# Kernel tuning notes

Hardware: AMD Instinct MI355X
Metric: run time of the kernel (lower is better)

The kernel has to match this reference:

```python
import jax, jax.numpy as jnp
import numpy as np
import math

STAGE_NUM = 10
K = 8
C = 256
KAPPA = 20.0


def _l2norm(x, axis):
    return x / (1e-06 + jnp.linalg.norm(x, axis=axis, keepdims=True))


def setup_inputs() -> dict:
    key = jax.random.key(0)
    k1, k2 = jax.random.split(key)
    support_feature = jax.random.normal(k1, (16, C, 128, 128), dtype=jnp.float32)
    mu = jax.random.normal(k2, (1, C, K), dtype=jnp.float32) * math.sqrt(2.0 / K)
    mu = _l2norm(mu, axis=1)  # matches mu.normal_(0, sqrt(2/k)) then _l2norm(dim=1)
    return {"support_feature": support_feature, "mu": mu}


def _em(x, mu0):
    # x: [b, c, n]; mu0: [b, c, k]
    b, c, n = x.shape

    def step(i, carry):
        mu, _ = carry
        # Kernel: kappa * x^T @ mu -> [b, n, k]
        z = jax.nn.softmax(KAPPA * jnp.einsum('bcn,bck->bnk', x, mu), axis=2)
        z_ = z / (1e-06 + z.sum(axis=1, keepdims=True))  # normalize over n
        mu = jnp.einsum('bcn,bnk->bck', x, z_)           # mu update
        mu = _l2norm(mu, axis=1)
        return (mu, z_)

    z_init = jnp.zeros((b, n, K), dtype=x.dtype)
    mu, z_ = jax.lax.fori_loop(0, STAGE_NUM, step, (mu0, z_init))
    return mu.transpose(0, 2, 1), z_  # mu: [b, k, c]


def reference(support_feature, mu):
    b, c, h, w = support_feature.shape
    x = support_feature.reshape(b, c, h * w)
    mu_b = jnp.broadcast_to(mu, (b, c, K))
    # Original runs EM entirely under torch.no_grad()
    mu_f, z_ = jax.lax.stop_gradient(_em(x, mu_b))
    # prototypes in original are list of mu_f[:, i, :, None, None]; return stacked mu_f
    return (mu_f, z_)
```

## Files before the change

### kernel.cpp

```cpp
#include <hip/hip_runtime.h>
#include <hip/hip_fp16.h>
#include <cstdint>
#include <cstddef>

#define NB 16
#define NC 256
#define NK 8
#define NN 16384
#define NSTAGE 10
#define FKAPPA 20.0f
#define NT 64
#define TPB 2
#define NBLK 128

__global__ __launch_bounds__(256) void k_init_mu(const float* __restrict__ mu_in,
                                                 float* __restrict__ mu_cur) {
    int i = blockIdx.x * 256 + threadIdx.x;
    mu_cur[i] = mu_in[i & (NC * NK - 1)];
}

template <bool WRITE_Z>
__global__ __launch_bounds__(256) void k_stage(const float* __restrict__ x,
                                               const float* __restrict__ mu,
                                               float* __restrict__ part,
                                               float* __restrict__ cspart,
                                               float* __restrict__ zraw) {
    const int b    = blockIdx.x >> 7;
    const int nt2  = blockIdx.x & (NBLK - 1);
    const int t    = threadIdx.x;
    const int lane = t & 63;
    const int wv   = t >> 6;

    __shared__ __align__(16) __half xt[NC][66];
    __shared__ __align__(16) float  smu[NC * NK];
    __shared__ __align__(16) float  dz[NT][12];

    for (int i = t; i < NC * NK; i += 256) smu[i] = mu[b * NC * NK + i];

    const int nl = (lane & 15) * 4;
    const int cg = lane >> 4;

    float a2[NK];
    float csk[NK];
    #pragma unroll
    for (int k = 0; k < NK; k++) { a2[k] = 0.f; csk[k] = 0.f; }

    for (int g = 0; g < TPB; ++g) {
        const int n0 = (nt2 * TPB + g) * NT;
        __syncthreads();
        if (t < NT * 12 / 4)
            reinterpret_cast<float4*>(dz)[t] = make_float4(0.f, 0.f, 0.f, 0.f);
        __syncthreads();

        const float* xp = x + (size_t)b * NC * NN + n0 + nl;
        float acc[4][NK];
        #pragma unroll
        for (int i = 0; i < 4; i++)
            #pragma unroll
            for (int k = 0; k < NK; k++) acc[i][k] = 0.f;

        #pragma unroll 8
        for (int ci = 0; ci < 16; ++ci) {
            const int c = wv * 64 + ci * 4 + cg;
            const float4 xv = *reinterpret_cast<const float4*>(xp + (size_t)c * NN);
            *reinterpret_cast<__half2*>(&xt[c][nl])     = __floats2half2_rn(xv.x, xv.y);
            *reinterpret_cast<__half2*>(&xt[c][nl + 2]) = __floats2half2_rn(xv.z, xv.w);
            const float4 m0 = *reinterpret_cast<const float4*>(&smu[c * NK]);
            const float4 m1 = *reinterpret_cast<const float4*>(&smu[c * NK + 4]);
            acc[0][0] += xv.x * m0.x; acc[0][1] += xv.x * m0.y; acc[0][2] += xv.x * m0.z; acc[0][3] += xv.x * m0.w;
            acc[0][4] += xv.x * m1.x; acc[0][5] += xv.x * m1.y; acc[0][6] += xv.x * m1.z; acc[0][7] += xv.x * m1.w;
            acc[1][0] += xv.y * m0.x; acc[1][1] += xv.y * m0.y; acc[1][2] += xv.y * m0.z; acc[1][3] += xv.y * m0.w;
            acc[1][4] += xv.y * m1.x; acc[1][5] += xv.y * m1.y; acc[1][6] += xv.y * m1.z; acc[1][7] += xv.y * m1.w;
            acc[2][0] += xv.z * m0.x; acc[2][1] += xv.z * m0.y; acc[2][2] += xv.z * m0.z; acc[2][3] += xv.z * m0.w;
            acc[2][4] += xv.z * m1.x; acc[2][5] += xv.z * m1.y; acc[2][6] += xv.z * m1.z; acc[2][7] += xv.z * m1.w;
            acc[3][0] += xv.w * m0.x; acc[3][1] += xv.w * m0.y; acc[3][2] += xv.w * m0.z; acc[3][3] += xv.w * m0.w;
            acc[3][4] += xv.w * m1.x; acc[3][5] += xv.w * m1.y; acc[3][6] += xv.w * m1.z; acc[3][7] += xv.w * m1.w;
        }

        #pragma unroll
        for (int m = 16; m <= 32; m <<= 1)
            #pragma unroll
            for (int i = 0; i < 4; i++)
                #pragma unroll
                for (int k = 0; k < NK; k++) acc[i][k] += __shfl_xor(acc[i][k], m, 64);

        if (lane < 16) {
            #pragma unroll
            for (int i = 0; i < 4; i++)
                #pragma unroll
                for (int k = 0; k < NK; k++) atomicAdd(&dz[nl + i][k], acc[i][k]);
        }
        __syncthreads();

        if (t < NT) {
            float l[NK];
            float mx = -1e30f;
            #pragma unroll
            for (int k = 0; k < NK; k++) { l[k] = FKAPPA * dz[t][k]; mx = fmaxf(mx, l[k]); }
            float s = 0.f;
            #pragma unroll
            for (int k = 0; k < NK; k++) { l[k] = __expf(l[k] - mx); s += l[k]; }
            const float inv = 1.f / s;
            #pragma unroll
            for (int k = 0; k < NK; k++) { l[k] *= inv; dz[t][k] = l[k]; }
            if (WRITE_Z) {
                float* zp = zraw + ((size_t)b * NN + n0 + t) * NK;
                *reinterpret_cast<float4*>(zp)     = make_float4(l[0], l[1], l[2], l[3]);
                *reinterpret_cast<float4*>(zp + 4) = make_float4(l[4], l[5], l[6], l[7]);
            }
            #pragma unroll
            for (int off = 32; off > 0; off >>= 1)
                #pragma unroll
                for (int k = 0; k < NK; k++) l[k] += __shfl_down(l[k], off, 64);
            #pragma unroll
            for (int k = 0; k < NK; k++) csk[k] += l[k];
        }
        __syncthreads();

        #pragma unroll 8
        for (int j = 0; j < NT / 2; ++j) {
            const __half2 xh = *reinterpret_cast<const __half2*>(&xt[t][2 * j]);
            const float2 xf = __half22float2(xh);
            const float4 za0 = *reinterpret_cast<const float4*>(&dz[2 * j][0]);
            const float4 za1 = *reinterpret_cast<const float4*>(&dz[2 * j][4]);
            const float4 zb0 = *reinterpret_cast<const float4*>(&dz[2 * j + 1][0]);
            const float4 zb1 = *reinterpret_cast<const float4*>(&dz[2 * j + 1][4]);
            a2[0] += xf.x * za0.x + xf.y * zb0.x;
            a2[1] += xf.x * za0.y + xf.y * zb0.y;
            a2[2] += xf.x * za0.z + xf.y * zb0.z;
            a2[3] += xf.x * za0.w + xf.y * zb0.w;
            a2[4] += xf.x * za1.x + xf.y * zb1.x;
            a2[5] += xf.x * za1.y + xf.y * zb1.y;
            a2[6] += xf.x * za1.z + xf.y * zb1.z;
            a2[7] += xf.x * za1.w + xf.y * zb1.w;
        }
    }

    float* pp = part + (size_t)blockIdx.x * (NC * NK) + t * NK;
    *reinterpret_cast<float4*>(pp)     = make_float4(a2[0], a2[1], a2[2], a2[3]);
    *reinterpret_cast<float4*>(pp + 4) = make_float4(a2[4], a2[5], a2[6], a2[7]);
    if (t == 0) {
        #pragma unroll
        for (int k = 0; k < NK; k++) cspart[blockIdx.x * NK + k] = csk[k];
    }
}

__global__ __launch_bounds__(256) void k_reduce(const float* __restrict__ part,
                                                const float* __restrict__ cspart,
                                                float* __restrict__ num,
                                                float* __restrict__ colsum) {
    const int b  = blockIdx.x >> 3;
    const int cg = blockIdx.x & 7;
    const int t  = threadIdx.x;
    const int ck = cg * 256 + t;

    float s = 0.f;
    const float* p = part + (size_t)b * NBLK * (NC * NK) + ck;
    #pragma unroll 8
    for (int g = 0; g < NBLK; ++g) s += p[(size_t)g * (NC * NK)];
    num[b * (NC * NK) + ck] = s;

    __shared__ float cred[2][NK];
    if (cg == 0 && t < NBLK) {
        const float4 u0 = *reinterpret_cast<const float4*>(&cspart[(b * NBLK + t) * NK]);
        const float4 u1 = *reinterpret_cast<const float4*>(&cspart[(b * NBLK + t) * NK + 4]);
        float v[NK] = {u0.x, u0.y, u0.z, u0.w, u1.x, u1.y, u1.z, u1.w};
        #pragma unroll
        for (int off = 32; off > 0; off >>= 1)
            #pragma unroll
            for (int k = 0; k < NK; k++) v[k] += __shfl_down(v[k], off, 64);
        if ((t & 63) == 0)
            #pragma unroll
            for (int k = 0; k < NK; k++) cred[t >> 6][k] = v[k];
    }
    __syncthreads();
    if (cg == 0 && t < NK) colsum[b * NK + t] = cred[0][t] + cred[1][t];
}

__global__ __launch_bounds__(256) void k_newmu(const float* __restrict__ num,
                                               const float* __restrict__ colsum,
                                               float* __restrict__ mu_out) {
    const int b = blockIdx.x;
    const int t = threadIdx.x;
    float inv[NK];
    #pragma unroll
    for (int k = 0; k < NK; k++) inv[k] = 1.f / (1e-6f + colsum[b * NK + k]);

    const float4 v0 = *reinterpret_cast<const float4*>(num + (size_t)b * NC * NK + t * NK);
    const float4 v1 = *reinterpret_cast<const float4*>(num + (size_t)b * NC * NK + t * NK + 4);
    float v[NK] = {v0.x * inv[0], v0.y * inv[1], v0.z * inv[2], v0.w * inv[3],
                   v1.x * inv[4], v1.y * inv[5], v1.z * inv[6], v1.w * inv[7]};

    float sq[NK];
    #pragma unroll
    for (int k = 0; k < NK; k++) sq[k] = v[k] * v[k];
    #pragma unroll
    for (int off = 32; off > 0; off >>= 1)
        #pragma unroll
        for (int k = 0; k < NK; k++) sq[k] += __shfl_down(sq[k], off, 64);

    __shared__ float red[4][NK];
    const int wave = t >> 6, lane = t & 63;
    if (lane == 0)
        #pragma unroll
        for (int k = 0; k < NK; k++) red[wave][k] = sq[k];
    __syncthreads();
    __shared__ float scale[NK];
    if (t < NK) {
        const float tot = red[0][t] + red[1][t] + red[2][t] + red[3][t];
        scale[t] = 1.f / (1e-6f + sqrtf(tot));
    }
    __syncthreads();
    #pragma unroll
    for (int k = 0; k < NK; k++) v[k] *= scale[k];
    *reinterpret_cast<float4*>(mu_out + (size_t)b * NC * NK + t * NK)     = make_float4(v[0], v[1], v[2], v[3]);
    *reinterpret_cast<float4*>(mu_out + (size_t)b * NC * NK + t * NK + 4) = make_float4(v[4], v[5], v[6], v[7]);
}

__global__ __launch_bounds__(256) void k_write_mu(const float* __restrict__ mu,
                                                  float* __restrict__ out) {
    const int i = blockIdx.x * 256 + threadIdx.x;
    const int b = i >> 11, r = i & 2047;
    const int k = r >> 8, c = r & 255;
    out[i] = mu[(size_t)b * NC * NK + c * NK + k];
}

__global__ __launch_bounds__(256) void k_write_z(const float* __restrict__ colsum,
                                                 float* __restrict__ out1) {
    const int i = blockIdx.x * 256 + threadIdx.x;
    const int b = i >> 12;
    const int n4 = (i & 4095) * 4;
    float inv[NK];
    #pragma unroll
    for (int k = 0; k < NK; k++) inv[k] = 1.f / (1e-6f + colsum[b * NK + k]);

    float4* p = reinterpret_cast<float4*>(out1 + ((size_t)b * NN + n4) * NK);
    #pragma unroll
    for (int j = 0; j < 4; ++j) {
        float4 a = p[2 * j], c = p[2 * j + 1];
        a.x *= inv[0]; a.y *= inv[1]; a.z *= inv[2]; a.w *= inv[3];
        c.x *= inv[4]; c.y *= inv[5]; c.z *= inv[6]; c.w *= inv[7];
        p[2 * j] = a; p[2 * j + 1] = c;
    }
}

extern "C" void kernel_launch(void* const* d_in, const int* in_sizes, int n_in,
                              void* d_out, int out_size, void* d_ws, size_t ws_size,
                              hipStream_t stream) {
    const float* x     = (const float*)d_in[0];
    const float* mu_in = (const float*)d_in[1];
    float* out  = (float*)d_out;
    float* out1 = out + NB * NK * NC;
    char* ws = (char*)d_ws;

    const size_t PART_BYTES = (size_t)NB * NBLK * NC * NK * 4;
    const size_t CSP_BYTES  = (size_t)NB * NBLK * NK * 4;
    const size_t NUM_BYTES  = (size_t)NB * NC * NK * 4;
    const size_t CS_BYTES   = (size_t)NB * NK * 4;

    float* part   = (float*)ws;
    float* cspart = (float*)(ws + PART_BYTES);
    float* num    = (float*)(ws + PART_BYTES + CSP_BYTES);
    float* colsum = (float*)(ws + PART_BYTES + CSP_BYTES + NUM_BYTES);
    float* mu_a   = (float*)(ws + PART_BYTES + CSP_BYTES + NUM_BYTES + CS_BYTES);

    k_init_mu<<<NB * NC * NK / 256, 256, 0, stream>>>(mu_in, mu_a);

    for (int s = 0; s < NSTAGE; ++s) {
        if (s == NSTAGE - 1)
            k_stage<true><<<NB * NBLK, 256, 0, stream>>>(x, mu_a, part, cspart, out1);
        else
            k_stage<false><<<NB * NBLK, 256, 0, stream>>>(x, mu_a, part, cspart, out1);
        k_reduce<<<NB * 8, 256, 0, stream>>>(part, cspart, num, colsum);
        k_newmu<<<NB, 256, 0, stream>>>(num, colsum, mu_a);
    }

    k_write_mu<<<NB * NK * NC / 256, 256, 0, stream>>>(mu_a, out);
    k_write_z<<<NB * NN / 4 / 256, 256, 0, stream>>>(colsum, out1);
}
```

Measured before the change: 1.688 ms.

## Double stage block to 512 threads, prefetch x loads, replace LDS atomics with per-wave partials

Each stage block now runs 512 threads (8 waves). Each wave covers 32 channels, and all eight float4 x loads are issued up front before the compute. The LDS atomicAdd reduction of logits is replaced by per-wave partial buffers that the softmax threads sum. The second matmul is split across two thread halves over n, which doubles the partial buffer and the reduce kernel's loop. This trades more LDS use and twice the reduction traffic for more memory parallelism and no atomics.

```diff
diff --git a/kernel.cpp b/kernel.cpp
--- a/kernel.cpp
+++ b/kernel.cpp
@@ -20,11 +20,11 @@
 }
 
 template <bool WRITE_Z>
-__global__ __launch_bounds__(256) void k_stage(const float* __restrict__ x,
-                                               const float* __restrict__ mu,
-                                               float* __restrict__ part,
-                                               float* __restrict__ cspart,
-                                               float* __restrict__ zraw) {
+__global__ __launch_bounds__(512, 4) void k_stage(const float* __restrict__ x,
+                                                  const float* __restrict__ mu,
+                                                  float* __restrict__ part,
+                                                  float* __restrict__ cspart,
+                                                  float* __restrict__ zraw) {
     const int b    = blockIdx.x >> 7;
     const int nt2  = blockIdx.x & (NBLK - 1);
     const int t    = threadIdx.x;
@@ -33,48 +33,53 @@
 
     __shared__ __align__(16) __half xt[NC][66];
     __shared__ __align__(16) float  smu[NC * NK];
+    __shared__ __align__(16) float  dzp[8][NT][9];
     __shared__ __align__(16) float  dz[NT][12];
 
-    for (int i = t; i < NC * NK; i += 256) smu[i] = mu[b * NC * NK + i];
+    reinterpret_cast<float4*>(smu)[t] =
+        reinterpret_cast<const float4*>(mu + (size_t)b * NC * NK)[t];
 
     const int nl = (lane & 15) * 4;
     const int cg = lane >> 4;
-
-    float a2[NK];
-    float csk[NK];
+    const int c2 = t & 255;
+    const int nh = t >> 8;
+
+    float a2[NK], csk[NK];
     #pragma unroll
     for (int k = 0; k < NK; k++) { a2[k] = 0.f; csk[k] = 0.f; }
 
     for (int g = 0; g < TPB; ++g) {
         const int n0 = (nt2 * TPB + g) * NT;
         __syncthreads();
-        if (t < NT * 12 / 4)
-            reinterpret_cast<float4*>(dz)[t] = make_float4(0.f, 0.f, 0.f, 0.f);
-        __syncthreads();
 
         const float* xp = x + (size_t)b * NC * NN + n0 + nl;
+        float4 xv[8];
+        #pragma unroll
+        for (int ci = 0; ci < 8; ++ci)
+            xv[ci] = *reinterpret_cast<const float4*>(xp + (size_t)(wv * 32 + ci * 4 + cg) * NN);
+
         float acc[4][NK];
         #pragma unroll
         for (int i = 0; i < 4; i++)
             #pragma unroll
             for (int k = 0; k < NK; k++) acc[i][k] = 0.f;
 
-        #pragma unroll 8
-        for (int ci = 0; ci < 16; ++ci) {
-            const int c = wv * 64 + ci * 4 + cg;
-            const float4 xv = *reinterpret_cast<const float4*>(xp + (size_t)c * NN);
-            *reinterpret_cast<__half2*>(&xt[c][nl])     = __floats2half2_rn(xv.x, xv.y);
-            *reinterpret_cast<__half2*>(&xt[c][nl + 2]) = __floats2half2_rn(xv.z, xv.w);
+        #pragma unroll
+        for (int ci = 0; ci < 8; ++ci) {
+            const int c = wv * 32 + ci * 4 + cg;
+            const float4 v = xv[ci];
+            *reinterpret_cast<__half2*>(&xt[c][nl])     = __floats2half2_rn(v.x, v.y);
+            *reinterpret_cast<__half2*>(&xt[c][nl + 2]) = __floats2half2_rn(v.z, v.w);
             const float4 m0 = *reinterpret_cast<const float4*>(&smu[c * NK]);
             const float4 m1 = *reinterpret_cast<const float4*>(&smu[c * NK + 4]);
-            acc[0][0] += xv.x * m0.x; acc[0][1] += xv.x * m0.y; acc[0][2] += xv.x * m0.z; acc[0][3] += xv.x * m0.w;
-            acc[0][4] += xv.x * m1.x; acc[0][5] += xv.x * m1.y; acc[0][6] += xv.x * m1.z; acc[0][7] += xv.x * m1.w;
-            acc[1][0] += xv.y * m0.x; acc[1][1] += xv.y * m0.y; acc[1][2] += xv.y * m0.z; acc[1][3] += xv.y * m0.w;
-            acc[1][4] += xv.y * m1.x; acc[1][5] += xv.y * m1.y; acc[1][6] += xv.y * m1.z; acc[1][7] += xv.y * m1.w;
-            acc[2][0] += xv.z * m0.x; acc[2][1] += xv.z * m0.y; acc[2][2] += xv.z * m0.z; acc[2][3] += xv.z * m0.w;
-            acc[2][4] += xv.z * m1.x; acc[2][5] += xv.z * m1.y; acc[2][6] += xv.z * m1.z; acc[2][7] += xv.z * m1.w;
-            acc[3][0] += xv.w * m0.x; acc[3][1] += xv.w * m0.y; acc[3][2] += xv.w * m0.z; acc[3][3] += xv.w * m0.w;
-            acc[3][4] += xv.w * m1.x; acc[3][5] += xv.w * m1.y; acc[3][6] += xv.w * m1.z; acc[3][7] += xv.w * m1.w;
+            acc[0][0] += v.x * m0.x; acc[0][1] += v.x * m0.y; acc[0][2] += v.x * m0.z; acc[0][3] += v.x * m0.w;
+            acc[0][4] += v.x * m1.x; acc[0][5] += v.x * m1.y; acc[0][6] += v.x * m1.z; acc[0][7] += v.x * m1.w;
+            acc[1][0] += v.y * m0.x; acc[1][1] += v.y * m0.y; acc[1][2] += v.y * m0.z; acc[1][3] += v.y * m0.w;
+            acc[1][4] += v.y * m1.x; acc[1][5] += v.y * m1.y; acc[1][6] += v.y * m1.z; acc[1][7] += v.y * m1.w;
+            acc[2][0] += v.z * m0.x; acc[2][1] += v.z * m0.y; acc[2][2] += v.z * m0.z; acc[2][3] += v.z * m0.w;
+            acc[2][4] += v.z * m1.x; acc[2][5] += v.z * m1.y; acc[2][6] += v.z * m1.z; acc[2][7] += v.z * m1.w;
+            acc[3][0] += v.w * m0.x; acc[3][1] += v.w * m0.y; acc[3][2] += v.w * m0.z; acc[3][3] += v.w * m0.w;
+            acc[3][4] += v.w * m1.x; acc[3][5] += v.w * m1.y; acc[3][6] += v.w * m1.z; acc[3][7] += v.w * m1.w;
         }
 
         #pragma unroll
@@ -88,7 +93,7 @@
             #pragma unroll
             for (int i = 0; i < 4; i++)
                 #pragma unroll
-                for (int k = 0; k < NK; k++) atomicAdd(&dz[nl + i][k], acc[i][k]);
+                for (int k = 0; k < NK; k++) dzp[wv][nl + i][k] = acc[i][k];
         }
         __syncthreads();
 
@@ -96,7 +101,13 @@
             float l[NK];
             float mx = -1e30f;
             #pragma unroll
-            for (int k = 0; k < NK; k++) { l[k] = FKAPPA * dz[t][k]; mx = fmaxf(mx, l[k]); }
+            for (int k = 0; k < NK; k++) {
+                float s = dzp[0][t][k];
+                #pragma unroll
+                for (int w = 1; w < 8; ++w) s += dzp[w][t][k];
+                l[k] = FKAPPA * s;
+                mx = fmaxf(mx, l[k]);
+            }
             float s = 0.f;
             #pragma unroll
             for (int k = 0; k < NK; k++) { l[k] = __expf(l[k] - mx); s += l[k]; }
@@ -118,8 +129,9 @@
         __syncthreads();
 
         #pragma unroll 8
-        for (int j = 0; j < NT / 2; ++j) {
-            const __half2 xh = *reinterpret_cast<const __half2*>(&xt[t][2 * j]);
+        for (int jj = 0; jj < 16; ++jj) {
+            const int j = nh * 16 + jj;
+            const __half2 xh = *reinterpret_cast<const __half2*>(&xt[c2][2 * j]);
             const float2 xf = __half22float2(xh);
             const float4 za0 = *reinterpret_cast<const float4*>(&dz[2 * j][0]);
             const float4 za1 = *reinterpret_cast<const float4*>(&dz[2 * j][4]);
@@ -136,7 +148,7 @@
         }
     }
 
-    float* pp = part + (size_t)blockIdx.x * (NC * NK) + t * NK;
+    float* pp = part + (size_t)blockIdx.x * (2 * NC * NK) + (size_t)nh * (NC * NK) + c2 * NK;
     *reinterpret_cast<float4*>(pp)     = make_float4(a2[0], a2[1], a2[2], a2[3]);
     *reinterpret_cast<float4*>(pp + 4) = make_float4(a2[4], a2[5], a2[6], a2[7]);
     if (t == 0) {
@@ -155,9 +167,9 @@
     const int ck = cg * 256 + t;
 
     float s = 0.f;
-    const float* p = part + (size_t)b * NBLK * (NC * NK) + ck;
+    const float* p = part + (size_t)b * NBLK * (2 * NC * NK) + ck;
     #pragma unroll 8
-    for (int g = 0; g < NBLK; ++g) s += p[(size_t)g * (NC * NK)];
+    for (int m = 0; m < 2 * NBLK; ++m) s += p[(size_t)m * (NC * NK)];
     num[b * (NC * NK) + ck] = s;
 
     __shared__ float cred[2][NK];
@@ -253,7 +265,7 @@
     float* out1 = out + NB * NK * NC;
     char* ws = (char*)d_ws;
 
-    const size_t PART_BYTES = (size_t)NB * NBLK * NC * NK * 4;
+    const size_t PART_BYTES = (size_t)NB * NBLK * 2 * NC * NK * 4;
     const size_t CSP_BYTES  = (size_t)NB * NBLK * NK * 4;
     const size_t NUM_BYTES  = (size_t)NB * NC * NK * 4;
     const size_t CS_BYTES   = (size_t)NB * NK * 4;
@@ -268,9 +280,9 @@
 
     for (int s = 0; s < NSTAGE; ++s) {
         if (s == NSTAGE - 1)
-            k_stage<true><<<NB * NBLK, 256, 0, stream>>>(x, mu_a, part, cspart, out1);
+            k_stage<true><<<NB * NBLK, 512, 0, stream>>>(x, mu_a, part, cspart, out1);
         else
-            k_stage<false><<<NB * NBLK, 256, 0, stream>>>(x, mu_a, part, cspart, out1);
+            k_stage<false><<<NB * NBLK, 512, 0, stream>>>(x, mu_a, part, cspart, out1);
         k_reduce<<<NB * 8, 256, 0, stream>>>(part, cspart, num, colsum);
         k_newmu<<<NB, 256, 0, stream>>>(num, colsum, mu_a);
     }
```

New measurement: 1.738 ms. +3.0%, slower.
